# Kernel tuning notes

Measured on AMD Instinct MI355X. Metric: run time of the kernel, lower is better.

Reference implementation:

```python
import jax, jax.numpy as jnp
import numpy as np

B, T, M, D, H, DH = 2, 2048, 2048, 384, 4, 96
NM, DF, R, NA = 8, 1536, 16, 4
S = 0.02  # weight init scale

PARAM_NAMES = ['cWq','cbq','cWk','cbk','cWv','cbv','cWo','cbo',
               'sWq','sbq','sWk','sbk','sWv','sbv','sWo','sbo',
               'gW','gb','f1W','f1b','f2W','f2b','adA','adB',
               'ln1g','ln1b','ln2g','ln2b','ln3g','ln3b']

def setup_inputs() -> dict:
    key = jax.random.key(0)
    ks = jax.random.split(key, 20)
    n = lambda k, sh, s=1.0: jax.random.normal(k, sh, dtype=jnp.float32) * s
    z = lambda sh: jnp.zeros(sh, dtype=jnp.float32)
    o = lambda sh: jnp.ones(sh, dtype=jnp.float32)
    return {
        'x': n(ks[0], (B, T, D)),
        'mem': n(ks[1], (B, M, D)),
        'motif_ctrl': n(ks[2], (B, NM)),
        'adapter_idx': 1,
        'cWq': n(ks[3], (D, D), S), 'cbq': z((D,)),
        'cWk': n(ks[4], (D, D), S), 'cbk': z((D,)),
        'cWv': n(ks[5], (D, D), S), 'cbv': z((D,)),
        'cWo': n(ks[6], (D, D), S), 'cbo': z((D,)),
        'sWq': n(ks[7], (D, D), S), 'sbq': z((D,)),
        'sWk': n(ks[8], (D, D), S), 'sbk': z((D,)),
        'sWv': n(ks[9], (D, D), S), 'sbv': z((D,)),
        'sWo': n(ks[10], (D, D), S), 'sbo': z((D,)),
        'gW': n(ks[11], (H, NM), S), 'gb': z((H,)),
        'f1W': n(ks[12], (DF, D), S), 'f1b': z((DF,)),
        'f2W': n(ks[13], (D, DF), S), 'f2b': z((D,)),
        'adA': n(ks[14], (NA, R, D), S),
        'adB': n(ks[15], (NA, D, R), S),
        'ln1g': o((D,)), 'ln1b': z((D,)),
        'ln2g': o((D,)), 'ln2b': z((D,)),
        'ln3g': o((D,)), 'ln3b': z((D,)),
    }

def _lin(x, W, b):
    return x @ W.T + b  # torch nn.Linear convention: W is [out, in]

def _layernorm(x, g, b):
    mu = x.mean(-1, keepdims=True)
    var = ((x - mu) ** 2).mean(-1, keepdims=True)
    return (x - mu) * jax.lax.rsqrt(var + 1e-5) * g + b

def _block(x, mem, motif_ctrl, adapter_idx, p):
    scale = 1.0 / np.sqrt(DH).astype(np.float32)
    # --- cross-attention over memory ---
    h = _layernorm(x, p['ln1g'], p['ln1b'])
    q = _lin(h, p['cWq'], p['cbq']).reshape(B, T, H, DH)
    k = _lin(mem, p['cWk'], p['cbk']).reshape(B, M, H, DH)
    v = _lin(mem, p['cWv'], p['cbv']).reshape(B, M, H, DH)
    A = jax.nn.softmax(jnp.einsum('bthd,bmhd->bhtm', q, k) * scale, axis=-1)
    z = jnp.einsum('bhtm,bmhd->bthd', A, v).reshape(B, T, D)
    x = x + _lin(z, p['cWo'], p['cbo'])
    # --- motif-gated self-attention (post-softmax per-head gate) ---
    h = _layernorm(x, p['ln2g'], p['ln2b'])
    gates = jax.nn.sigmoid(motif_ctrl @ p['gW'].T + p['gb'])  # [B, H]
    q = _lin(h, p['sWq'], p['sbq']).reshape(B, T, H, DH)
    k = _lin(h, p['sWk'], p['sbk']).reshape(B, T, H, DH)
    v = _lin(h, p['sWv'], p['sbv']).reshape(B, T, H, DH)
    A = jax.nn.softmax(jnp.einsum('bthd,bshd->bhts', q, k) * scale, axis=-1)
    A = A * gates[:, :, None, None]
    z = jnp.einsum('bhts,bshd->bthd', A, v).reshape(B, T, D)
    x = x + _lin(z, p['sWo'], p['sbo'])
    # --- LoRA-adapter FFN ---
    h = _layernorm(x, p['ln3g'], p['ln3b'])
    f = _lin(jax.nn.gelu(_lin(h, p['f1W'], p['f1b']), approximate=False), p['f2W'], p['f2b'])
    f = f + (h @ p['adA'][adapter_idx].T) @ p['adB'][adapter_idx].T
    return x + f

def reference(x, mem, motif_ctrl, adapter_idx,
              cWq, cbq, cWk, cbk, cWv, cbv, cWo, cbo,
              sWq, sbq, sWk, sbk, sWv, sbv, sWo, sbo,
              gW, gb, f1W, f1b, f2W, f2b, adA, adB,
              ln1g, ln1b, ln2g, ln2b, ln3g, ln3b):
    p = dict(zip(PARAM_NAMES, (cWq, cbq, cWk, cbk, cWv, cbv, cWo, cbo,
                               sWq, sbq, sWk, sbk, sWv, sbv, sWo, sbo,
                               gW, gb, f1W, f1b, f2W, f2b, adA, adB,
                               ln1g, ln1b, ln2g, ln2b, ln3g, ln3b)))
    return _block(x, mem, motif_ctrl, int(adapter_idx), p)
```

## Files before the change

kernel.cpp:

```cpp
#include <hip/hip_runtime.h>
#include <hip/hip_bf16.h>
#include <math.h>

#define B_   2
#define T_   2048
#define M_   2048
#define D_   384
#define H_   4
#define DH_  96
#define NM_  8
#define DF_  1536
#define R_   16
#define NR_  4096

typedef unsigned short u16;
typedef u16    u16x8  __attribute__((ext_vector_type(8)));
typedef u16    u16x4  __attribute__((ext_vector_type(4)));
typedef __bf16 bf16x8 __attribute__((ext_vector_type(8)));
typedef float  f32x4  __attribute__((ext_vector_type(4)));

union V8 { u16x8 u; bf16x8 b; };
__device__ __forceinline__ bf16x8 as_bf(u16x8 x) { V8 v; v.u = x; return v.b; }

__device__ __forceinline__ u16 f2bf(float f) {
    unsigned u = __float_as_uint(f);
    unsigned r = (u + 0x7fffu + ((u >> 16) & 1u)) >> 16;
    return (u16)r;
}

__device__ __forceinline__ void load16(const u16* g, u16* l) {
    __builtin_amdgcn_global_load_lds(
        (const __attribute__((address_space(1))) void*)g,
        (__attribute__((address_space(3))) void*)l, 16, 0, 0);
}

__global__ __launch_bounds__(256)
void setup_kernel(const float* cWq, const float* cWk, const float* cWv, const float* cWo,
                  const float* sWq, const float* sWk, const float* sWv, const float* sWo,
                  const float* f1W, const float* f2W, const float* adA, const float* adB,
                  const float* mem,
                  u16* Wq_c, u16* Wkv_c, u16* Wco, u16* Wqkv_s, u16* Wso,
                  u16* Wf1, u16* Wf2, u16* WadA, u16* WadB, u16* memb,
                  const float* cbk, const float* cbv,
                  const float* sbq, const float* sbk, const float* sbv,
                  float* bkv_c, float* bqkv_s,
                  const float* mc, const float* gW, const float* gb, float* gates) {
    int seg = blockIdx.y;
    if (seg == 13) {
        for (int i = blockIdx.x * 256 + threadIdx.x; i < 1928; i += gridDim.x * 256) {
            if (i < 768) bkv_c[i] = (i < 384) ? cbk[i] : cbv[i - 384];
            else if (i < 1920) {
                int j = i - 768;
                bqkv_s[j] = (j < 384) ? sbq[j] : (j < 768 ? sbk[j - 384] : sbv[j - 768]);
            } else {
                int k = i - 1920;
                int b = k / H_, h = k % H_;
                float s = gb[h];
                for (int n = 0; n < NM_; n++)
                    s += mc[b * NM_ + n] * gW[h * NM_ + n];
                gates[k] = 1.f / (1.f + __expf(-s));
            }
        }
        return;
    }
    const float* s; u16* d; int n;
    switch (seg) {
        case 0:  s = cWq; d = Wq_c;            n = 147456; break;
        case 1:  s = cWk; d = Wkv_c;           n = 147456; break;
        case 2:  s = cWv; d = Wkv_c + 147456;  n = 147456; break;
        case 3:  s = cWo; d = Wco;             n = 147456; break;
        case 4:  s = sWq; d = Wqkv_s;          n = 147456; break;
        case 5:  s = sWk; d = Wqkv_s + 147456; n = 147456; break;
        case 6:  s = sWv; d = Wqkv_s + 294912; n = 147456; break;
        case 7:  s = sWo; d = Wso;             n = 147456; break;
        case 8:  s = f1W; d = Wf1;             n = 589824; break;
        case 9:  s = f2W; d = Wf2;             n = 589824; break;
        case 10: s = adA; d = WadA;            n = 24576;  break;
        case 11: s = adB; d = WadB;            n = 24576;  break;
        default: s = mem; d = memb;            n = 1572864; break;
    }
    for (int i = blockIdx.x * 256 + threadIdx.x; i < n; i += gridDim.x * 256)
        d[i] = f2bf(s[i]);
}

__global__ __launch_bounds__(384)
void ln_kernel(const float* __restrict__ x, const float* __restrict__ g,
               const float* __restrict__ b, u16* __restrict__ out) {
    __shared__ float sm[8];
    int row = blockIdx.x;
    int t = threadIdx.x;
    float v = x[(long)row * D_ + t];

    float s = v;
    for (int o = 32; o > 0; o >>= 1) s += __shfl_down(s, o);
    if ((t & 63) == 0) sm[t >> 6] = s;
    __syncthreads();
    float mu = 0.f;
    for (int i = 0; i < 6; i++) mu += sm[i];
    mu *= (1.f / D_);
    __syncthreads();

    float d = v - mu;
    s = d * d;
    for (int o = 32; o > 0; o >>= 1) s += __shfl_down(s, o);
    if ((t & 63) == 0) sm[t >> 6] = s;
    __syncthreads();
    float var = 0.f;
    for (int i = 0; i < 6; i++) var += sm[i];
    var *= (1.f / D_);

    float r = rsqrtf(var + 1e-5f);
    out[(long)row * D_ + t] = f2bf(d * r * g[t] + b[t]);
}

template<int ACT, bool OBF, bool VT, bool LORA>
__global__ __launch_bounds__(256)
void gemm_pipe(const u16* __restrict__ A, const u16* __restrict__ W,
               const float* __restrict__ bias, const float* __restrict__ res,
               void* __restrict__ Cout, int NC, int K,
               u16* __restrict__ Vt, int vtbase,
               const u16* __restrict__ Tl, const u16* __restrict__ adB,
               const int* __restrict__ aidx) {
    __shared__ __align__(16) u16 As[8192];
    __shared__ __align__(16) u16 Ws[8192];
    int tid = threadIdx.x, w = tid >> 6, lane = tid & 63;
    int l15 = lane & 15, quad = lane >> 4;
    int bm = blockIdx.y * 64, bn = blockIdx.x * 64;
    int mt0 = (w & 1) * 2, nt0 = (w >> 1) * 2;

    const u16* Ag[2]; const u16* Wg[2]; u16* Al[2]; u16* Wl[2];
    #pragma unroll
    for (int s = 0; s < 2; s++) {
        int r = s * 4 + w, mt = r >> 1, kc = r & 1;
        Ag[s] = A + (long)(bm + mt * 16 + l15) * K + kc * 32 + quad * 8;
        Wg[s] = W + (long)(bn + mt * 16 + l15) * K + kc * 32 + quad * 8;
        Al[s] = As + r * 512;
        Wl[s] = Ws + r * 512;
    }

    f32x4 acc[2][2];
    #pragma unroll
    for (int i = 0; i < 2; i++)
        #pragma unroll
        for (int j = 0; j < 2; j++) acc[i][j] = (f32x4){0.f, 0.f, 0.f, 0.f};

    int niter = K >> 6;
    #pragma unroll
    for (int s = 0; s < 2; s++) { load16(Ag[s], Al[s]); load16(Wg[s], Wl[s]); }

    for (int i = 0; i < niter; i++) {
        __syncthreads();
        int cur = (i & 1) * 4096, nxt = 4096 - cur;
        if (i + 1 < niter) {
            int k = (i + 1) << 6;
            #pragma unroll
            for (int s = 0; s < 2; s++) {
                load16(Ag[s] + k, Al[s] + nxt);
                load16(Wg[s] + k, Wl[s] + nxt);
            }
        }
        #pragma unroll
        for (int kc = 0; kc < 2; kc++) {
            u16x8 af[2], bfv[2];
            #pragma unroll
            for (int s = 0; s < 2; s++) {
                af[s]  = *(const u16x8*)(As + cur + ((mt0 + s) * 2 + kc) * 512 + lane * 8);
                bfv[s] = *(const u16x8*)(Ws + cur + ((nt0 + s) * 2 + kc) * 512 + lane * 8);
            }
            #pragma unroll
            for (int s = 0; s < 2; s++)
                #pragma unroll
                for (int j = 0; j < 2; j++)
                    acc[s][j] = __builtin_amdgcn_mfma_f32_16x16x32_bf16(
                        as_bf(af[s]), as_bf(bfv[j]), acc[s][j], 0, 0, 0);
        }
    }

    if (LORA) {
        long aoff = (long)aidx[0] * 6144;
        u16x8 tlf[2] = {{0,0,0,0,0,0,0,0}, {0,0,0,0,0,0,0,0}};
        u16x8 adf[2] = {{0,0,0,0,0,0,0,0}, {0,0,0,0,0,0,0,0}};
        #pragma unroll
        for (int s = 0; s < 2; s++) {
            if (quad < 2) {
                tlf[s] = *(const u16x8*)(Tl + (long)(bm + (mt0 + s) * 16 + l15) * 16 + quad * 8);
                adf[s] = *(const u16x8*)(adB + aoff + (long)(bn + (nt0 + s) * 16 + l15) * 16 + quad * 8);
            }
        }
        #pragma unroll
        for (int s = 0; s < 2; s++)
            #pragma unroll
            for (int j = 0; j < 2; j++)
                acc[s][j] = __builtin_amdgcn_mfma_f32_16x16x32_bf16(
                    as_bf(tlf[s]), as_bf(adf[j]), acc[s][j], 0, 0, 0);
    }

    #pragma unroll
    for (int mi = 0; mi < 2; mi++) {
        #pragma unroll
        for (int nj = 0; nj < 2; nj++) {
            int col = bn + (nt0 + nj) * 16 + l15;
            float bv = bias ? bias[col] : 0.f;
            int rowb = bm + (mt0 + mi) * 16 + quad * 4;
            if (VT && col >= vtbase) {
                int vc = col - vtbase;
                int b = rowb >> 11, rowl = rowb & 2047;
                u16x4 ov;
                #pragma unroll
                for (int r = 0; r < 4; r++) ov[r] = f2bf(acc[mi][nj][r] + bv);
                *(u16x4*)(Vt + ((long)b * 384 + vc) * 2048 + rowl) = ov;
            } else {
                #pragma unroll
                for (int r = 0; r < 4; r++) {
                    float v = acc[mi][nj][r] + bv;
                    if (ACT == 1) v = 0.5f * v * (1.f + erff(v * 0.70710678118654752f));
                    long idx = (long)(rowb + r) * NC + col;
                    if (res) v += res[idx];
                    if (OBF) ((u16*)Cout)[idx] = f2bf(v);
                    else     ((float*)Cout)[idx] = v;
                }
            }
        }
    }
}

template<int ACT, bool OBF>
__global__ __launch_bounds__(256)
void gemm_small(const u16* __restrict__ A, const u16* __restrict__ W,
                const float* __restrict__ bias, const float* __restrict__ res,
                void* __restrict__ Cout, int NR, int NC, int K,
                const int* __restrict__ aidx, int astride) {
    if (aidx) W += (long)aidx[0] * astride;
    __shared__ __align__(16) u16 As[2048];
    __shared__ __align__(16) u16 Ws[2048];
    int tid = threadIdx.x;
    int w = tid >> 6, lane = tid & 63;
    int bm = blockIdx.y * 64, bn = blockIdx.x * 64;
    int mt0 = (w & 1) * 2, nt0 = (w >> 1) * 2;

    int srow = ((tid >> 6) << 4) + (tid & 15);
    int kq8  = ((tid >> 4) & 3) * 8;
    const u16* Ag = A + (long)(bm + srow) * K + kq8;
    int wrow = bn + srow;
    const u16* Wg = W + (long)wrow * K + kq8;
    bool wok = wrow < NC;

    f32x4 acc[2][2];
    #pragma unroll
    for (int i = 0; i < 2; i++)
        #pragma unroll
        for (int j = 0; j < 2; j++) acc[i][j] = (f32x4){0.f, 0.f, 0.f, 0.f};

    for (int k0 = 0; k0 < K; k0 += 32) {
        u16x8 av = {0, 0, 0, 0, 0, 0, 0, 0};
        u16x8 wv = {0, 0, 0, 0, 0, 0, 0, 0};
        bool kok = (k0 + kq8) < K;
        if (kok) av = *(const u16x8*)(Ag + k0);
        if (kok && wok) wv = *(const u16x8*)(Wg + k0);
        __syncthreads();
        *(u16x8*)(As + tid * 8) = av;
        *(u16x8*)(Ws + tid * 8) = wv;
        __syncthreads();
        u16x8 af[2], bfv[2];
        #pragma unroll
        for (int i = 0; i < 2; i++) {
            af[i]  = *(const u16x8*)(As + (mt0 + i) * 512 + lane * 8);
            bfv[i] = *(const u16x8*)(Ws + (nt0 + i) * 512 + lane * 8);
        }
        #pragma unroll
        for (int i = 0; i < 2; i++)
            #pragma unroll
            for (int j = 0; j < 2; j++)
                acc[i][j] = __builtin_amdgcn_mfma_f32_16x16x32_bf16(
                    as_bf(af[i]), as_bf(bfv[j]), acc[i][j], 0, 0, 0);
    }

    int quad = lane >> 4, l15 = lane & 15;
    #pragma unroll
    for (int mi = 0; mi < 2; mi++) {
        #pragma unroll
        for (int nj = 0; nj < 2; nj++) {
            int col = bn + (nt0 + nj) * 16 + l15;
            if (col < NC) {
                float bv = bias ? bias[col] : 0.f;
                int rowb = bm + (mt0 + mi) * 16 + quad * 4;
                #pragma unroll
                for (int r = 0; r < 4; r++) {
                    float v = acc[mi][nj][r] + bv;
                    if (ACT == 1) v = 0.5f * v * (1.f + erff(v * 0.70710678118654752f));
                    long idx = (long)(rowb + r) * NC + col;
                    if (res) v += res[idx];
                    if (OBF) ((u16*)Cout)[idx] = f2bf(v);
                    else     ((float*)Cout)[idx] = v;
                }
            }
        }
    }
}

__global__ __launch_bounds__(256)
void attn_mfma(const u16* __restrict__ Qg, int qs,
               const u16* __restrict__ Kg, int ks,
               const u16* __restrict__ Vt,
               float* __restrict__ Po, float* __restrict__ Pl) {
    __shared__ __align__(16) u16 Ks[6144];
    __shared__ __align__(16) u16 Vs[6144];
    __shared__ __align__(16) u16 Ps[4 * 1088];
    const float SCALE = 0.10206207261596575f;

    int tid = threadIdx.x, wv = tid >> 6, lane = tid & 63;
    int l15 = lane & 15, quad = lane >> 4;
    int bh = blockIdx.y, b = bh >> 2, h = bh & 3;
    int split = blockIdx.z;
    int q0 = blockIdx.x * 64 + wv * 16;

    const u16* Qb = Qg + (long)(b * 2048 + q0) * qs + h * 96;
    const u16* Kb = Kg + (long)(b * 2048 + split * 512) * ks + h * 96;
    const u16* Vb = Vt + (long)(b * 384 + h * 96) * 2048 + split * 512;

    u16x8 qf[3];
    #pragma unroll
    for (int t = 0; t < 3; t++)
        qf[t] = *(const u16x8*)(Qb + (long)l15 * qs + t * 32 + quad * 8);

    f32x4 o[6];
    #pragma unroll
    for (int i = 0; i < 6; i++) o[i] = (f32x4){0.f, 0.f, 0.f, 0.f};
    float rs[4] = {0.f, 0.f, 0.f, 0.f};
    u16* Pw = Ps + wv * 1088;

    const u16* KgI[3]; u16* KlI[3]; const u16* VgI[3]; u16* VlI[3];
    #pragma unroll
    for (int i = 0; i < 3; i++) {
        int r = i * 4 + wv;
        int ksub = r & 3, kst = r >> 2;
        KgI[i] = Kb + (long)(ksub * 16 + l15) * ks + kst * 32 + quad * 8;
        KlI[i] = Ks + (ksub * 3 + kst) * 512;
        int nt = r >> 1, t2 = r & 1;
        VgI[i] = Vb + (long)(nt * 16 + l15) * 2048 + t2 * 32 + quad * 8;
        VlI[i] = Vs + r * 512;
    }

    for (int j0 = 0; j0 < 512; j0 += 64) {
        __syncthreads();
        #pragma unroll
        for (int i = 0; i < 3; i++) {
            load16(KgI[i] + (long)j0 * ks, KlI[i]);
            load16(VgI[i] + j0, VlI[i]);
        }
        __syncthreads();

        f32x4 sc[4];
        #pragma unroll
        for (int s = 0; s < 4; s++) sc[s] = (f32x4){0.f, 0.f, 0.f, 0.f};
        #pragma unroll
        for (int s = 0; s < 4; s++)
            #pragma unroll
            for (int t = 0; t < 3; t++) {
                u16x8 kf = *(const u16x8*)(Ks + (s * 3 + t) * 512 + lane * 8);
                sc[s] = __builtin_amdgcn_mfma_f32_16x16x32_bf16(as_bf(qf[t]), as_bf(kf), sc[s], 0, 0, 0);
            }

        #pragma unroll
        for (int s = 0; s < 4; s++) {
            int base = (s >> 1) * 544 + ((((s & 1) << 1) | (l15 >> 3))) * 136 + (l15 & 7);
            #pragma unroll
            for (int r = 0; r < 4; r++) {
                float p = __expf(sc[s][r] * SCALE);
                rs[r] += p;
                Pw[base + (quad * 4 + r) * 8] = f2bf(p);
            }
        }
        #pragma unroll
        for (int t2 = 0; t2 < 2; t2++) {
            u16x8 pf = *(const u16x8*)(Pw + t2 * 544 + quad * 136 + l15 * 8);
            #pragma unroll
            for (int nt = 0; nt < 6; nt++) {
                u16x8 vf = *(const u16x8*)(Vs + (nt * 2 + t2) * 512 + lane * 8);
                o[nt] = __builtin_amdgcn_mfma_f32_16x16x32_bf16(as_bf(pf), as_bf(vf), o[nt], 0, 0, 0);
            }
        }
    }

    #pragma unroll
    for (int off = 1; off < 16; off <<= 1)
        #pragma unroll
        for (int r = 0; r < 4; r++) rs[r] += __shfl_xor(rs[r], off);

    float* Pob = Po + ((long)(split * 8 + bh) * 2048 + q0) * 96;
    #pragma unroll
    for (int nt = 0; nt < 6; nt++)
        #pragma unroll
        for (int r = 0; r < 4; r++)
            Pob[(long)(quad * 4 + r) * 96 + nt * 16 + l15] = o[nt][r];
    if (l15 == 0) {
        long mb = (long)(split * 8 + bh) * 2048 + q0 + quad * 4;
        #pragma unroll
        for (int r = 0; r < 4; r++) Pl[mb + r] = rs[r];
    }
}

__global__ __launch_bounds__(256)
void attn_combine(const float* __restrict__ Po, const float* __restrict__ Pl,
                  const float* __restrict__ gates, u16* __restrict__ Z) {
    int bh = blockIdx.y, b = bh >> 2, h = bh & 3;
    int tid = threadIdx.x;
    int rl = tid >> 2, part = tid & 3;
    int row = blockIdx.x * 64 + rl;
    long rbase = (long)bh * 2048 + row;

    float L = 0.f;
    #pragma unroll
    for (int s = 0; s < 4; s++) L += Pl[s * 16384 + rbase];
    float g = gates ? gates[bh] : 1.f;
    float sc = g / L;

    u16* Zr = Z + ((long)(b * 2048) + row) * 384 + h * 96 + part * 24;
    #pragma unroll
    for (int i = 0; i < 24; i += 4) {
        f32x4 acc = (f32x4){0.f, 0.f, 0.f, 0.f};
        #pragma unroll
        for (int s = 0; s < 4; s++) {
            f32x4 v = *(const f32x4*)(Po + ((long)s * 16384 + rbase) * 96 + part * 24 + i);
            #pragma unroll
            for (int e = 0; e < 4; e++) acc[e] += v[e];
        }
        u16x4 ov;
        #pragma unroll
        for (int e = 0; e < 4; e++) ov[e] = f2bf(acc[e] * sc);
        *(u16x4*)(Zr + i) = ov;
    }
}

extern "C" void kernel_launch(void* const* d_in, const int* in_sizes, int n_in,
                              void* d_out, int out_size, void* d_ws, size_t ws_size,
                              hipStream_t stream) {
    const float* x    = (const float*)d_in[0];
    const float* mem  = (const float*)d_in[1];
    const float* mc   = (const float*)d_in[2];
    const int*   aidx = (const int*)d_in[3];
    const float* cWq = (const float*)d_in[4],  *cbq = (const float*)d_in[5];
    const float* cWk = (const float*)d_in[6],  *cbk = (const float*)d_in[7];
    const float* cWv = (const float*)d_in[8],  *cbv = (const float*)d_in[9];
    const float* cWo = (const float*)d_in[10], *cbo = (const float*)d_in[11];
    const float* sWq = (const float*)d_in[12], *sbq = (const float*)d_in[13];
    const float* sWk = (const float*)d_in[14], *sbk = (const float*)d_in[15];
    const float* sWv = (const float*)d_in[16], *sbv = (const float*)d_in[17];
    const float* sWo = (const float*)d_in[18], *sbo = (const float*)d_in[19];
    const float* gW  = (const float*)d_in[20], *gb  = (const float*)d_in[21];
    const float* f1W = (const float*)d_in[22], *f1b = (const float*)d_in[23];
    const float* f2W = (const float*)d_in[24], *f2b = (const float*)d_in[25];
    const float* adA = (const float*)d_in[26], *adB = (const float*)d_in[27];
    const float* ln1g = (const float*)d_in[28], *ln1b = (const float*)d_in[29];
    const float* ln2g = (const float*)d_in[30], *ln2b = (const float*)d_in[31];
    const float* ln3g = (const float*)d_in[32], *ln3b = (const float*)d_in[33];

    u16* p = (u16*)d_ws;
    u16* H      = p; p += (size_t)NR_ * 384;
    u16* bufQ   = p; p += (size_t)NR_ * 384;
    u16* bufKV  = p; p += (size_t)NR_ * 768;
    u16* bufQKV = p; p += (size_t)NR_ * 1152;
    u16* Vt     = p; p += (size_t)B_ * 384 * 2048;
    u16* Zb     = p; p += (size_t)NR_ * 384;
    u16* F      = p; p += (size_t)NR_ * 1536;
    u16* Tl     = p; p += (size_t)NR_ * 16;
    u16* memb   = p; p += (size_t)NR_ * 384;
    u16* Wq_c   = p; p += 147456;
    u16* Wkv_c  = p; p += 294912;
    u16* Wco    = p; p += 147456;
    u16* Wqkv_s = p; p += 442368;
    u16* Wso    = p; p += 147456;
    u16* Wf1    = p; p += 589824;
    u16* Wf2    = p; p += 589824;
    u16* WadA   = p; p += 24576;
    u16* WadB   = p; p += 24576;
    float* fp = (float*)p;
    float* X1 = fp;     fp += (size_t)NR_ * 384;
    float* X2 = fp;     fp += (size_t)NR_ * 384;
    float* Po = fp;     fp += (size_t)4 * 8 * 2048 * 96;
    float* Pl = fp;     fp += (size_t)4 * 8 * 2048;
    float* bkv_c  = fp; fp += 768;
    float* bqkv_s = fp; fp += 1152;
    float* gbuf   = fp; fp += 8;

    setup_kernel<<<dim3(96, 14), 256, 0, stream>>>(
        cWq, cWk, cWv, cWo, sWq, sWk, sWv, sWo, f1W, f2W, adA, adB, mem,
        Wq_c, Wkv_c, Wco, Wqkv_s, Wso, Wf1, Wf2, WadA, WadB, memb,
        cbk, cbv, sbq, sbk, sbv, bkv_c, bqkv_s, mc, gW, gb, gbuf);

    const float* nf = nullptr;
    const u16* nu = nullptr;
    ln_kernel<<<NR_, 384, 0, stream>>>(x, ln1g, ln1b, H);
    gemm_pipe<0, true, false, false><<<dim3(6, 64), 256, 0, stream>>>(H, Wq_c, cbq, nf, bufQ, 384, 384, nullptr, 0, nu, nu, nullptr);
    gemm_pipe<0, true, true, false><<<dim3(12, 64), 256, 0, stream>>>(memb, Wkv_c, bkv_c, nf, bufKV, 768, 384, Vt, 384, nu, nu, nullptr);
    attn_mfma<<<dim3(32, 8, 4), 256, 0, stream>>>(bufQ, 384, bufKV, 768, Vt, Po, Pl);
    attn_combine<<<dim3(32, 8), 256, 0, stream>>>(Po, Pl, nullptr, Zb);
    gemm_pipe<0, false, false, false><<<dim3(6, 64), 256, 0, stream>>>(Zb, Wco, cbo, x, X1, 384, 384, nullptr, 0, nu, nu, nullptr);

    ln_kernel<<<NR_, 384, 0, stream>>>(X1, ln2g, ln2b, H);
    gemm_pipe<0, true, true, false><<<dim3(18, 64), 256, 0, stream>>>(H, Wqkv_s, bqkv_s, nf, bufQKV, 1152, 384, Vt, 768, nu, nu, nullptr);
    attn_mfma<<<dim3(32, 8, 4), 256, 0, stream>>>(bufQKV, 1152, bufQKV + 384, 1152, Vt, Po, Pl);
    attn_combine<<<dim3(32, 8), 256, 0, stream>>>(Po, Pl, gbuf, Zb);
    gemm_pipe<0, false, false, false><<<dim3(6, 64), 256, 0, stream>>>(Zb, Wso, sbo, X1, X2, 384, 384, nullptr, 0, nu, nu, nullptr);

    ln_kernel<<<NR_, 384, 0, stream>>>(X2, ln3g, ln3b, H);
    gemm_pipe<1, true, false, false><<<dim3(24, 64), 256, 0, stream>>>(H, Wf1, f1b, nf, F, 1536, 384, nullptr, 0, nu, nu, nullptr);
    gemm_small<0, true><<<dim3(1, 64), 256, 0, stream>>>(H, WadA, nullptr, nf, Tl, NR_, 16, 384, aidx, R_ * D_);
    gemm_pipe<0, false, false, true><<<dim3(6, 64), 256, 0, stream>>>(F, Wf2, f2b, X2, d_out, 384, 1536, nullptr, 0, Tl, WadB, aidx);
}
```

Measured before the change: 380.7 us.

## Double-buffer K/V tiles and process two query groups per wave in attention

The attention kernel now keeps two LDS buffers for K and V. The next 64-key tile is prefetched while the current one is consumed, which removes one barrier per iteration. Each wave also handles 32 query rows (two 16-row groups) instead of 16, so every K/V fragment read from LDS feeds two MFMAs, and the grid is halved. In exchange, LDS use and register pressure rise and fewer blocks launch, which may lower occupancy.

```diff
diff --git a/kernel.cpp b/kernel.cpp
--- a/kernel.cpp
+++ b/kernel.cpp
@@ -303,81 +303,101 @@
                const u16* __restrict__ Kg, int ks,
                const u16* __restrict__ Vt,
                float* __restrict__ Po, float* __restrict__ Pl) {
-    __shared__ __align__(16) u16 Ks[6144];
-    __shared__ __align__(16) u16 Vs[6144];
-    __shared__ __align__(16) u16 Ps[4 * 1088];
+    __shared__ __align__(16) u16 Ks[2][6144];
+    __shared__ __align__(16) u16 Vs[2][6144];
+    __shared__ __align__(16) u16 Ps[4][2][1088];
     const float SCALE = 0.10206207261596575f;
 
     int tid = threadIdx.x, wv = tid >> 6, lane = tid & 63;
     int l15 = lane & 15, quad = lane >> 4;
     int bh = blockIdx.y, b = bh >> 2, h = bh & 3;
     int split = blockIdx.z;
-    int q0 = blockIdx.x * 64 + wv * 16;
+    int q0 = blockIdx.x * 128 + wv * 32;
 
     const u16* Qb = Qg + (long)(b * 2048 + q0) * qs + h * 96;
     const u16* Kb = Kg + (long)(b * 2048 + split * 512) * ks + h * 96;
     const u16* Vb = Vt + (long)(b * 384 + h * 96) * 2048 + split * 512;
 
-    u16x8 qf[3];
-    #pragma unroll
-    for (int t = 0; t < 3; t++)
-        qf[t] = *(const u16x8*)(Qb + (long)l15 * qs + t * 32 + quad * 8);
-
-    f32x4 o[6];
-    #pragma unroll
-    for (int i = 0; i < 6; i++) o[i] = (f32x4){0.f, 0.f, 0.f, 0.f};
-    float rs[4] = {0.f, 0.f, 0.f, 0.f};
-    u16* Pw = Ps + wv * 1088;
-
-    const u16* KgI[3]; u16* KlI[3]; const u16* VgI[3]; u16* VlI[3];
+    u16x8 qf[2][3];
+    #pragma unroll
+    for (int g = 0; g < 2; g++)
+        #pragma unroll
+        for (int t = 0; t < 3; t++)
+            qf[g][t] = *(const u16x8*)(Qb + (long)(g * 16 + l15) * qs + t * 32 + quad * 8);
+
+    f32x4 o[2][6];
+    #pragma unroll
+    for (int g = 0; g < 2; g++)
+        #pragma unroll
+        for (int i = 0; i < 6; i++) o[g][i] = (f32x4){0.f, 0.f, 0.f, 0.f};
+    float rs[2][4] = {{0.f, 0.f, 0.f, 0.f}, {0.f, 0.f, 0.f, 0.f}};
+
+    const u16* KgI[3]; int KlO[3]; const u16* VgI[3]; int VlO[3];
     #pragma unroll
     for (int i = 0; i < 3; i++) {
         int r = i * 4 + wv;
         int ksub = r & 3, kst = r >> 2;
         KgI[i] = Kb + (long)(ksub * 16 + l15) * ks + kst * 32 + quad * 8;
-        KlI[i] = Ks + (ksub * 3 + kst) * 512;
+        KlO[i] = (ksub * 3 + kst) * 512;
         int nt = r >> 1, t2 = r & 1;
         VgI[i] = Vb + (long)(nt * 16 + l15) * 2048 + t2 * 32 + quad * 8;
-        VlI[i] = Vs + r * 512;
-    }
-
-    for (int j0 = 0; j0 < 512; j0 += 64) {
+        VlO[i] = r * 512;
+    }
+
+    #pragma unroll
+    for (int i = 0; i < 3; i++) {
+        load16(KgI[i], &Ks[0][0] + KlO[i]);
+        load16(VgI[i], &Vs[0][0] + VlO[i]);
+    }
+
+    for (int it = 0; it < 8; it++) {
         __syncthreads();
-        #pragma unroll
-        for (int i = 0; i < 3; i++) {
-            load16(KgI[i] + (long)j0 * ks, KlI[i]);
-            load16(VgI[i] + j0, VlI[i]);
-        }
-        __syncthreads();
-
-        f32x4 sc[4];
-        #pragma unroll
-        for (int s = 0; s < 4; s++) sc[s] = (f32x4){0.f, 0.f, 0.f, 0.f};
+        int cur = it & 1, nxt = cur ^ 1;
+        if (it + 1 < 8) {
+            int j = (it + 1) * 64;
+            #pragma unroll
+            for (int i = 0; i < 3; i++) {
+                load16(KgI[i] + (long)j * ks, &Ks[nxt][0] + KlO[i]);
+                load16(VgI[i] + j, &Vs[nxt][0] + VlO[i]);
+            }
+        }
+
+        f32x4 sc[2][4];
+        #pragma unroll
+        for (int g = 0; g < 2; g++)
+            #pragma unroll
+            for (int s = 0; s < 4; s++) sc[g][s] = (f32x4){0.f, 0.f, 0.f, 0.f};
         #pragma unroll
         for (int s = 0; s < 4; s++)
             #pragma unroll
             for (int t = 0; t < 3; t++) {
-                u16x8 kf = *(const u16x8*)(Ks + (s * 3 + t) * 512 + lane * 8);
-                sc[s] = __builtin_amdgcn_mfma_f32_16x16x32_bf16(as_bf(qf[t]), as_bf(kf), sc[s], 0, 0, 0);
-            }
-
-        #pragma unroll
-        for (int s = 0; s < 4; s++) {
-            int base = (s >> 1) * 544 + ((((s & 1) << 1) | (l15 >> 3))) * 136 + (l15 & 7);
-            #pragma unroll
-            for (int r = 0; r < 4; r++) {
-                float p = __expf(sc[s][r] * SCALE);
-                rs[r] += p;
-                Pw[base + (quad * 4 + r) * 8] = f2bf(p);
-            }
-        }
+                u16x8 kf = *(const u16x8*)(&Ks[cur][0] + (s * 3 + t) * 512 + lane * 8);
+                sc[0][s] = __builtin_amdgcn_mfma_f32_16x16x32_bf16(as_bf(qf[0][t]), as_bf(kf), sc[0][s], 0, 0, 0);
+                sc[1][s] = __builtin_amdgcn_mfma_f32_16x16x32_bf16(as_bf(qf[1][t]), as_bf(kf), sc[1][s], 0, 0, 0);
+            }
+
+        #pragma unroll
+        for (int g = 0; g < 2; g++)
+            #pragma unroll
+            for (int s = 0; s < 4; s++) {
+                int base = (s >> 1) * 544 + ((((s & 1) << 1) | (l15 >> 3))) * 136 + (l15 & 7);
+                #pragma unroll
+                for (int r = 0; r < 4; r++) {
+                    float p = __expf(sc[g][s][r] * SCALE);
+                    rs[g][r] += p;
+                    Ps[wv][g][base + (quad * 4 + r) * 8] = f2bf(p);
+                }
+            }
+
         #pragma unroll
         for (int t2 = 0; t2 < 2; t2++) {
-            u16x8 pf = *(const u16x8*)(Pw + t2 * 544 + quad * 136 + l15 * 8);
+            u16x8 pf0 = *(const u16x8*)(&Ps[wv][0][0] + t2 * 544 + quad * 136 + l15 * 8);
+            u16x8 pf1 = *(const u16x8*)(&Ps[wv][1][0] + t2 * 544 + quad * 136 + l15 * 8);
             #pragma unroll
             for (int nt = 0; nt < 6; nt++) {
-                u16x8 vf = *(const u16x8*)(Vs + (nt * 2 + t2) * 512 + lane * 8);
-                o[nt] = __builtin_amdgcn_mfma_f32_16x16x32_bf16(as_bf(pf), as_bf(vf), o[nt], 0, 0, 0);
+                u16x8 vf = *(const u16x8*)(&Vs[cur][0] + (nt * 2 + t2) * 512 + lane * 8);
+                o[0][nt] = __builtin_amdgcn_mfma_f32_16x16x32_bf16(as_bf(pf0), as_bf(vf), o[0][nt], 0, 0, 0);
+                o[1][nt] = __builtin_amdgcn_mfma_f32_16x16x32_bf16(as_bf(pf1), as_bf(vf), o[1][nt], 0, 0, 0);
             }
         }
     }
@@ -385,18 +405,23 @@
     #pragma unroll
     for (int off = 1; off < 16; off <<= 1)
         #pragma unroll
-        for (int r = 0; r < 4; r++) rs[r] += __shfl_xor(rs[r], off);
-
-    float* Pob = Po + ((long)(split * 8 + bh) * 2048 + q0) * 96;
-    #pragma unroll
-    for (int nt = 0; nt < 6; nt++)
-        #pragma unroll
-        for (int r = 0; r < 4; r++)
-            Pob[(long)(quad * 4 + r) * 96 + nt * 16 + l15] = o[nt][r];
-    if (l15 == 0) {
-        long mb = (long)(split * 8 + bh) * 2048 + q0 + quad * 4;
-        #pragma unroll
-        for (int r = 0; r < 4; r++) Pl[mb + r] = rs[r];
+        for (int g = 0; g < 2; g++)
+            #pragma unroll
+            for (int r = 0; r < 4; r++) rs[g][r] += __shfl_xor(rs[g][r], off);
+
+    #pragma unroll
+    for (int g = 0; g < 2; g++) {
+        float* Pob = Po + ((long)(split * 8 + bh) * 2048 + q0 + g * 16) * 96;
+        #pragma unroll
+        for (int nt = 0; nt < 6; nt++)
+            #pragma unroll
+            for (int r = 0; r < 4; r++)
+                Pob[(long)(quad * 4 + r) * 96 + nt * 16 + l15] = o[g][nt][r];
+        if (l15 == 0) {
+            long mb = (long)(split * 8 + bh) * 2048 + q0 + g * 16 + quad * 4;
+            #pragma unroll
+            for (int r = 0; r < 4; r++) Pl[mb + r] = rs[g][r];
+        }
     }
 }
 
@@ -493,13 +518,13 @@
     ln_kernel<<<NR_, 384, 0, stream>>>(x, ln1g, ln1b, H);
     gemm_pipe<0, true, false, false><<<dim3(6, 64), 256, 0, stream>>>(H, Wq_c, cbq, nf, bufQ, 384, 384, nullptr, 0, nu, nu, nullptr);
     gemm_pipe<0, true, true, false><<<dim3(12, 64), 256, 0, stream>>>(memb, Wkv_c, bkv_c, nf, bufKV, 768, 384, Vt, 384, nu, nu, nullptr);
-    attn_mfma<<<dim3(32, 8, 4), 256, 0, stream>>>(bufQ, 384, bufKV, 768, Vt, Po, Pl);
+    attn_mfma<<<dim3(16, 8, 4), 256, 0, stream>>>(bufQ, 384, bufKV, 768, Vt, Po, Pl);
     attn_combine<<<dim3(32, 8), 256, 0, stream>>>(Po, Pl, nullptr, Zb);
     gemm_pipe<0, false, false, false><<<dim3(6, 64), 256, 0, stream>>>(Zb, Wco, cbo, x, X1, 384, 384, nullptr, 0, nu, nu, nullptr);
 
     ln_kernel<<<NR_, 384, 0, stream>>>(X1, ln2g, ln2b, H);
     gemm_pipe<0, true, true, false><<<dim3(18, 64), 256, 0, stream>>>(H, Wqkv_s, bqkv_s, nf, bufQKV, 1152, 384, Vt, 768, nu, nu, nullptr);
-    attn_mfma<<<dim3(32, 8, 4), 256, 0, stream>>>(bufQKV, 1152, bufQKV + 384, 1152, Vt, Po, Pl);
+    attn_mfma<<<dim3(16, 8, 4), 256, 0, stream>>>(bufQKV, 1152, bufQKV + 384, 1152, Vt, Po, Pl);
     attn_combine<<<dim3(32, 8), 256, 0, stream>>>(Po, Pl, gbuf, Zb);
     gemm_pipe<0, false, false, false><<<dim3(6, 64), 256, 0, stream>>>(Zb, Wso, sbo, X1, X2, 384, 384, nullptr, 0, nu, nu, nullptr);
 
```

Result: faster. 371.6 us (-2.4%).
